# Performance work log

Hardware: AMD Instinct MI355X
Metric: run time of the kernel (lower is better)

Reference implementation:

```python
import jax, jax.numpy as jnp
import numpy as np

N_NODES = 100000
N_EDGES = 1600000
IN_CH = 6
EDGE_FEAT = 8


def glorot(key, shape):
    lim = np.sqrt(6.0 / (shape[0] + shape[1]))
    return jax.random.uniform(key, shape, jnp.float32, -lim, lim)


def setup_inputs() -> dict:
    key = jax.random.key(0)
    ks = jax.random.split(key, 10)
    x = jax.random.normal(ks[0], (N_NODES, IN_CH), jnp.float32)
    edge_index = jax.random.randint(ks[1], (2, N_EDGES), 0, N_NODES, jnp.int64)
    edge_attr = jax.random.normal(ks[2], (N_EDGES, EDGE_FEAT), jnp.float32)
    return {
        "x": x,
        "edge_index": edge_index,
        "edge_attr": edge_attr,
        "W1": glorot(ks[3], (IN_CH, 32)), "b1": jnp.zeros((32,), jnp.float32),
        "W2": glorot(ks[4], (32, 16)), "b2": jnp.zeros((16,), jnp.float32),
        "W3": glorot(ks[5], (16 * 2 + EDGE_FEAT, 32)), "b3": jnp.zeros((32,), jnp.float32),
        "W4": glorot(ks[6], (32, 1)), "b4": jnp.zeros((1,), jnp.float32),
    }


def gcn_conv(x, src, dst, W, b, n_nodes):
    # PyG GCNConv: add self-loops, symmetric deg^{-1/2} normalization,
    # linear transform, scatter-add aggregation over incoming edges, bias.
    h = x @ W  # [N, out]
    deg = jnp.zeros((n_nodes,), h.dtype).at[dst].add(1.0) + 1.0  # +1 self-loop
    dinv = jax.lax.rsqrt(deg)  # [N]
    norm = dinv[src] * dinv[dst]  # [E]
    msg = h[src] * norm[:, None]  # gather + scale
    agg = jnp.zeros_like(h).at[dst].add(msg)
    agg = agg + h * (dinv * dinv)[:, None]  # self-loop term
    return agg + b


def reference(x, edge_index, edge_attr, W1, b1, W2, b2, W3, b3, W4, b4):
    src, dst = edge_index[0], edge_index[1]
    n = x.shape[0]
    h = jax.nn.relu(gcn_conv(x, src, dst, W1, b1, n))
    h = jax.nn.relu(gcn_conv(h, src, dst, W2, b2, n))
    # edge gather-concat-MLP
    edge_input = jnp.concatenate([h[src], h[dst], edge_attr], axis=1)  # [E, 40]
    out = jax.nn.relu(edge_input @ W3 + b3) @ W4 + b4  # [E, 1]
    return out.squeeze(-1)
```

## Files before the change

kernel.cpp:

```cpp
#include <hip/hip_runtime.h>


constexpr int TPB = 256;
constexpr int NB = 256;
constexpr int BSH = 8;
constexpr int MAXB = 1024;
constexpr int EDGE_ITERS = 4;

using short8  = __attribute__((ext_vector_type(8))) short;
using f32x16  = __attribute__((ext_vector_type(16))) float;
using uintx4  = __attribute__((ext_vector_type(4))) unsigned;
using floatx4 = __attribute__((ext_vector_type(4))) float;

__device__ __forceinline__ void nt_store4(uint4 v, uint4* p) {
    uintx4 e = {v.x, v.y, v.z, v.w};
    __builtin_nontemporal_store(e, reinterpret_cast<uintx4*>(p));
}
__device__ __forceinline__ float4 nt_load_f4(const float4* p) {
    floatx4 e = __builtin_nontemporal_load(reinterpret_cast<const floatx4*>(p));
    return float4{e.x, e.y, e.z, e.w};
}

__device__ __forceinline__ float bf_lo(unsigned w) {
    return __builtin_bit_cast(float, (unsigned)(w << 16));
}
__device__ __forceinline__ float bf_hi(unsigned w) {
    return __builtin_bit_cast(float, w & 0xFFFF0000u);
}
__device__ __forceinline__ unsigned bf1(float f) {
    unsigned u = __builtin_bit_cast(unsigned, f);
    return (u + 0x7FFFu + ((u >> 16) & 1u)) >> 16;
}
__device__ __forceinline__ unsigned pk(float lo, float hi) {
    return bf1(lo) | (bf1(hi) << 16);
}
__device__ __forceinline__ void unp8(uint4 v, float* o) {
    o[0] = bf_lo(v.x); o[1] = bf_hi(v.x); o[2] = bf_lo(v.y); o[3] = bf_hi(v.y);
    o[4] = bf_lo(v.z); o[5] = bf_hi(v.z); o[6] = bf_lo(v.w); o[7] = bf_hi(v.w);
}
__device__ __forceinline__ void unp6(uint4 v, float* o) {
    o[0] = bf_lo(v.x); o[1] = bf_hi(v.x); o[2] = bf_lo(v.y); o[3] = bf_hi(v.y);
    o[4] = bf_lo(v.z); o[5] = bf_hi(v.z);
}

__global__ void k_bhist(const int* __restrict__ dst, unsigned* __restrict__ histG,
                        int E, int B, int CH) {
    __shared__ unsigned h[MAXB];
    for (int t = threadIdx.x; t < B; t += blockDim.x) h[t] = 0;
    __syncthreads();
    int b = blockIdx.x;
    int beg = b * CH, end = min(E, beg + CH);
    for (int i = beg + threadIdx.x; i < end; i += blockDim.x)
        atomicAdd(&h[__builtin_nontemporal_load(dst + i) >> BSH], 1u);
    __syncthreads();
    for (int t = threadIdx.x; t < B; t += blockDim.x) histG[b * B + t] = h[t];
}

__global__ void k_scan1t(const unsigned* __restrict__ histG, unsigned* __restrict__ bsum,
                         int M, int B) {
    __shared__ unsigned s[TPB];
    int tid = threadIdx.x;
    int i = blockIdx.x * TPB + tid;
    unsigned v = (i < M) ? histG[(i % NB) * B + (i / NB)] : 0u;
    s[tid] = v;
    __syncthreads();
    for (int ofs = TPB / 2; ofs > 0; ofs >>= 1) {
        if (tid < ofs) s[tid] += s[tid + ofs];
        __syncthreads();
    }
    if (tid == 0) bsum[blockIdx.x] = s[0];
}

__global__ void k_scan2(unsigned* __restrict__ bsum, int nb) {
    __shared__ unsigned s[512];
    int tid = threadIdx.x;
    unsigned v = (tid < nb) ? bsum[tid] : 0u;
    s[tid] = v;
    __syncthreads();
    for (int ofs = 1; ofs < 512; ofs <<= 1) {
        unsigned t = (tid >= ofs) ? s[tid - ofs] : 0u;
        __syncthreads();
        s[tid] += t;
        __syncthreads();
    }
    if (tid < nb) bsum[tid] = s[tid] - v;
}

__global__ void k_scan3t(const unsigned* __restrict__ histG, const unsigned* __restrict__ bsum,
                         unsigned* __restrict__ scannedM, int M, int B) {
    __shared__ unsigned s[TPB];
    int tid = threadIdx.x;
    int i = blockIdx.x * TPB + tid;
    unsigned v = (i < M) ? histG[(i % NB) * B + (i / NB)] : 0u;
    s[tid] = v;
    __syncthreads();
    for (int ofs = 1; ofs < TPB; ofs <<= 1) {
        unsigned t = (tid >= ofs) ? s[tid - ofs] : 0u;
        __syncthreads();
        s[tid] += t;
        __syncthreads();
    }
    if (i < M) scannedM[i] = bsum[blockIdx.x] + s[tid] - v;
}

__global__ void k_bscatter(const int* __restrict__ src, const int* __restrict__ dst,
                           const unsigned* __restrict__ scannedM, unsigned* __restrict__ lvl1,
                           int E, int B, int CH) {
    __shared__ unsigned cur[MAXB];
    int b = blockIdx.x;
    for (int t = threadIdx.x; t < B; t += blockDim.x) cur[t] = scannedM[t * NB + b];
    __syncthreads();
    int beg = b * CH, end = min(E, beg + CH);
    for (int i = beg + threadIdx.x; i < end; i += blockDim.x) {
        int d = __builtin_nontemporal_load(dst + i);
        int sv = __builtin_nontemporal_load(src + i);
        int bk = d >> BSH;
        unsigned p = atomicAdd(&cur[bk], 1u);
        lvl1[p] = ((unsigned)sv << BSH) | (unsigned)(d & ((1 << BSH) - 1));
    }
}

__global__ void k_bbuild(const unsigned* __restrict__ lvl1, const unsigned* __restrict__ scannedM,
                         const float* __restrict__ x, unsigned* __restrict__ rowptr,
                         float* __restrict__ dinv, uint4* __restrict__ xs,
                         int* __restrict__ csr_src, int N, int E, int B) {
    __shared__ unsigned cnt[1 << BSH];
    __shared__ unsigned ro[1 << BSH];
    int b = blockIdx.x;
    int tid = threadIdx.x;
    unsigned gbase = scannedM[(size_t)b * NB];
    unsigned gend = (b + 1 < B) ? scannedM[(size_t)(b + 1) * NB] : (unsigned)E;
    cnt[tid] = 0;
    __syncthreads();
    for (unsigned i = gbase + tid; i < gend; i += (unsigned)blockDim.x)
        atomicAdd(&cnt[lvl1[i] & ((1u << BSH) - 1u)], 1u);
    __syncthreads();
    unsigned v = cnt[tid];
    ro[tid] = v;
    __syncthreads();
    for (int ofs = 1; ofs < (1 << BSH); ofs <<= 1) {
        unsigned t = (tid >= ofs) ? ro[tid - ofs] : 0u;
        __syncthreads();
        ro[tid] += t;
        __syncthreads();
    }
    unsigned excl = ro[tid] - v;
    int n = (b << BSH) + tid;
    if (n < N) {
        rowptr[n] = gbase + excl;
        float di = rsqrtf((float)v + 1.0f);
        dinv[n] = di;
        const float* xr = x + (size_t)n * 6;
        uint4 o;
        o.x = pk(xr[0] * di, xr[1] * di);
        o.y = pk(xr[2] * di, xr[3] * di);
        o.z = pk(xr[4] * di, xr[5] * di);
        o.w = 0u;
        xs[n] = o;
        if (n == N - 1) rowptr[N] = gend;
    }
    __syncthreads();
    cnt[tid] = gbase + excl;
    __syncthreads();
    for (unsigned i = gbase + tid; i < gend; i += (unsigned)blockDim.x) {
        unsigned w = lvl1[i];
        unsigned p = atomicAdd(&cnt[w & ((1u << BSH) - 1u)], 1u);
        csr_src[p] = (int)(w >> BSH);
    }
}

__global__ void k_gagg6f(const unsigned* __restrict__ rowptr, const int* __restrict__ csr_src,
                         const float* __restrict__ dinv, const uint4* __restrict__ xs,
                         const float* __restrict__ W1, const float* __restrict__ b1,
                         const float* __restrict__ W2, uint4* __restrict__ hs2, int N) {
    int gid = blockIdx.x * blockDim.x + threadIdx.x;
    int n = gid >> 2, q = gid & 3;
    if (n >= N) return;
    unsigned beg = rowptr[n], end = rowptr[n + 1];
    float acc[6] = {0.f, 0.f, 0.f, 0.f, 0.f, 0.f};
    for (unsigned j = beg + q; j < end; j += 4) {
        int s = __builtin_nontemporal_load(csr_src + j);
        float t[6];
        unp6(xs[s], t);
#pragma unroll
        for (int i = 0; i < 6; ++i) acc[i] += t[i];
    }
#pragma unroll
    for (int i = 0; i < 6; ++i) {
        acc[i] += __shfl_xor(acc[i], 1);
        acc[i] += __shfl_xor(acc[i], 2);
    }
    float t6[6];
    unp6(xs[n], t6);
#pragma unroll
    for (int i = 0; i < 6; ++i) acc[i] += t6[i];
    float di = dinv[n];
    float h1[8];
#pragma unroll
    for (int cc = 0; cc < 8; ++cc) {
        int oc = q * 8 + cc;
        float s = 0.f;
#pragma unroll
        for (int k = 0; k < 6; ++k) s = fmaf(acc[k], W1[k * 32 + oc], s);
        h1[cc] = fmaxf(fmaf(s, di, b1[oc]), 0.f);
    }
    float z[16];
#pragma unroll
    for (int j = 0; j < 16; ++j) z[j] = 0.f;
#pragma unroll
    for (int cc = 0; cc < 8; ++cc) {
        int c = q * 8 + cc;
        float a = h1[cc];
#pragma unroll
        for (int j = 0; j < 16; ++j) z[j] = fmaf(a, W2[c * 16 + j], z[j]);
    }
#pragma unroll
    for (int j = 0; j < 16; ++j) {
        z[j] += __shfl_xor(z[j], 1);
        z[j] += __shfl_xor(z[j], 2);
    }
    if (q < 2) {
        unsigned w[4];
#pragma unroll
        for (int p = 0; p < 4; ++p)
            w[p] = pk(z[q * 8 + 2 * p] * di, z[q * 8 + 2 * p + 1] * di);
        nt_store4(uint4{w[0], w[1], w[2], w[3]}, hs2 + (size_t)n * 2 + q);
    }
}

__global__ void k_gagg16(const unsigned* __restrict__ rowptr, const int* __restrict__ csr_src,
                         const float* __restrict__ dinv, const uint4* __restrict__ hs2,
                         const float* __restrict__ b2, uint4* __restrict__ h2, int N) {
    int gid = blockIdx.x * blockDim.x + threadIdx.x;
    int n = gid >> 3, q = gid & 7;
    int h = q & 1, e4 = q >> 1;
    if (n >= N) return;
    unsigned beg = rowptr[n], end = rowptr[n + 1];
    float acc[8] = {0.f, 0.f, 0.f, 0.f, 0.f, 0.f, 0.f, 0.f};
    for (unsigned j = beg + e4; j < end; j += 4) {
        int s = __builtin_nontemporal_load(csr_src + j);
        float t[8];
        unp8(hs2[(size_t)s * 2 + h], t);
#pragma unroll
        for (int i = 0; i < 8; ++i) acc[i] += t[i];
    }
#pragma unroll
    for (int i = 0; i < 8; ++i) {
        acc[i] += __shfl_xor(acc[i], 2);
        acc[i] += __shfl_xor(acc[i], 4);
    }
    if (e4) return;
    float t8[8];
    unp8(hs2[(size_t)n * 2 + h], t8);
    float di = dinv[n];
    unsigned w[4];
#pragma unroll
    for (int i = 0; i < 4; ++i) {
        float r0 = fmaxf(fmaf(acc[2 * i] + t8[2 * i], di, b2[h * 8 + 2 * i]), 0.f);
        float r1 = fmaxf(fmaf(acc[2 * i + 1] + t8[2 * i + 1], di, b2[h * 8 + 2 * i + 1]), 0.f);
        w[i] = pk(r0, r1);
    }
    h2[(size_t)n * 2 + h] = uint4{w[0], w[1], w[2], w[3]};
}

__global__ void k_wprep(const float* __restrict__ W3, const float* __restrict__ b3,
                        uint4* __restrict__ w3tab) {
    int lane = threadIdx.x;
    if (lane >= 64) return;
    int j = lane & 31, hi = lane >> 5;
#pragma unroll
    for (int s = 0; s < 3; ++s) {
        unsigned w[4];
#pragma unroll
        for (int p = 0; p < 4; ++p) {
            int k0 = s * 16 + hi * 8 + 2 * p;
            float f0 = (k0 < 40) ? W3[k0 * 32 + j] : (k0 == 40 ? b3[j] : 0.f);
            float f1 = (k0 + 1 < 40) ? W3[(k0 + 1) * 32 + j] : 0.f;
            w[p] = pk(f0, f1);
        }
        w3tab[lane * 3 + s] = uint4{w[0], w[1], w[2], w[3]};
    }
}

__global__ void __launch_bounds__(TPB) k_edge_mfma(
    const int* __restrict__ src, const int* __restrict__ dst,
    const uint4* __restrict__ h2, const float* __restrict__ eattr,
    const uint4* __restrict__ w3tab, const float* __restrict__ W4,
    const float* __restrict__ b4, float* __restrict__ out, int E) {
    const int lane = threadIdx.x & 63;
    const int wave = threadIdx.x >> 6;
    const int e31 = lane & 31;
    const int hi = lane >> 5;

    short8 wA0, wA1, wA2;
    {
        const uint4* wt = w3tab + (size_t)lane * 3;
        wA0 = __builtin_bit_cast(short8, wt[0]);
        wA1 = __builtin_bit_cast(short8, wt[1]);
        wA2 = __builtin_bit_cast(short8, wt[2]);
    }
    const float4* W4v = reinterpret_cast<const float4*>(W4);
    const float4 w4q0 = W4v[hi], w4q1 = W4v[2 + hi], w4q2 = W4v[4 + hi], w4q3 = W4v[6 + hi];
    const float b4v = b4[0];
    const long base0 = ((long)blockIdx.x * 4 + wave) * (32L * EDGE_ITERS);

    const uint4 one_u = (hi == 1) ? uint4{0x3F80u, 0u, 0u, 0u} : uint4{0u, 0u, 0u, 0u};
    const short8 one_s8 = __builtin_bit_cast(short8, one_u);

    auto eclamp = [&](int it) -> size_t {
        long et = base0 + (long)it * 32 + e31;
        return (size_t)(et < E ? et : (long)(E - 1));
    };
    auto load_a2 = [&](int it) -> short8 {
        if (hi != 0) return one_s8;
        const float4* ea = reinterpret_cast<const float4*>(eattr + eclamp(it) * 8);
        float4 e0 = nt_load_f4(ea);
        float4 e1 = nt_load_f4(ea + 1);
        return __builtin_bit_cast(short8, uint4{pk(e0.x, e0.y), pk(e0.z, e0.w),
                                                pk(e1.x, e1.y), pk(e1.z, e1.w)});
    };

    int is[EDGE_ITERS], id[EDGE_ITERS];
#pragma unroll
    for (int it = 0; it < EDGE_ITERS; ++it) {
        is[it] = __builtin_nontemporal_load(src + eclamp(it));
        id[it] = __builtin_nontemporal_load(dst + eclamp(it));
    }

    uint4 hsA = h2[(size_t)is[0] * 2 + hi], hdA = h2[(size_t)id[0] * 2 + hi];
    short8 a2A = load_a2(0);
    uint4 hsB = h2[(size_t)is[1] * 2 + hi], hdB = h2[(size_t)id[1] * 2 + hi];
    short8 a2B = load_a2(1);

#pragma unroll
    for (int it = 0; it < EDGE_ITERS; ++it) {
        uint4 hsC{0u, 0u, 0u, 0u}, hdC{0u, 0u, 0u, 0u};
        short8 a2C = one_s8;
        if (it + 2 < EDGE_ITERS) {
            hsC = h2[(size_t)is[it + 2] * 2 + hi];
            hdC = h2[(size_t)id[it + 2] * 2 + hi];
            a2C = load_a2(it + 2);
        }

        f32x16 c;
#pragma unroll
        for (int i = 0; i < 16; ++i) c[i] = 0.f;
        c = __builtin_amdgcn_mfma_f32_32x32x16_bf16(wA0, __builtin_bit_cast(short8, hsA), c, 0, 0, 0);
        c = __builtin_amdgcn_mfma_f32_32x32x16_bf16(wA1, __builtin_bit_cast(short8, hdA), c, 0, 0, 0);
        c = __builtin_amdgcn_mfma_f32_32x32x16_bf16(wA2, a2A, c, 0, 0, 0);

        float z = 0.f;
#pragma unroll
        for (int r = 0; r < 4; ++r) {
            z = fmaf(fmaxf(c[0 * 4 + r], 0.f), ((const float*)&w4q0)[r], z);
            z = fmaf(fmaxf(c[1 * 4 + r], 0.f), ((const float*)&w4q1)[r], z);
            z = fmaf(fmaxf(c[2 * 4 + r], 0.f), ((const float*)&w4q2)[r], z);
            z = fmaf(fmaxf(c[3 * 4 + r], 0.f), ((const float*)&w4q3)[r], z);
        }
        z += __shfl_xor(z, 32);
        long erow = base0 + (long)it * 32 + e31;
        if (hi == 0 && erow < E) __builtin_nontemporal_store(z + b4v, out + erow);

        hsA = hsB; hdA = hdB; a2A = a2B;
        hsB = hsC; hdB = hdC; a2B = a2C;
    }
}

extern "C" void kernel_launch(void* const* d_in, const int* in_sizes, int n_in,
                              void* d_out, int out_size, void* d_ws, size_t ws_size,
                              hipStream_t stream) {
    const float* x     = (const float*)d_in[0];
    const int*   ei    = (const int*)d_in[1];
    const float* eattr = (const float*)d_in[2];
    const float* W1 = (const float*)d_in[3];
    const float* b1 = (const float*)d_in[4];
    const float* W2 = (const float*)d_in[5];
    const float* b2 = (const float*)d_in[6];
    const float* W3 = (const float*)d_in[7];
    const float* b3 = (const float*)d_in[8];
    const float* W4 = (const float*)d_in[9];
    const float* b4 = (const float*)d_in[10];
    float* out = (float*)d_out;

    const int N = in_sizes[0] / 6;
    const int E = in_sizes[2] / 8;
    const int* src = ei;
    const int* dst = ei + E;

    const int B  = (N + (1 << BSH) - 1) >> BSH;
    const int CH = (E + NB - 1) / NB;
    const int M  = B * NB;
    const int nbM = (M + TPB - 1) / TPB;

    char* wsb = (char*)d_ws;
    size_t off = 0;
    auto alloc4 = [&](size_t elems) {
        void* p = wsb + off;
        off += ((elems * 4 + 15) & ~(size_t)15);
        return p;
    };
    unsigned* rowptr   = (unsigned*)alloc4(N + 1);
    float*    dinv     = (float*)alloc4(N);
    unsigned* bsum     = (unsigned*)alloc4(512);
    unsigned* histG    = (unsigned*)alloc4((size_t)NB * B);
    unsigned* scannedM = (unsigned*)alloc4((size_t)NB * B);
    int*      csr_src  = (int*)alloc4(E);
    unsigned* big      = (unsigned*)alloc4((size_t)N * 16 > (size_t)E ? (size_t)N * 16 : (size_t)E);
    uint4*    xs       = (uint4*)alloc4((size_t)N * 4);
    uint4*    w3tab    = (uint4*)alloc4(64 * 3 * 4);

    unsigned* lvl1 = big;
    uint4*    hs2  = (uint4*)big;
    uint4*    h2   = (uint4*)(big + (size_t)N * 8);

    k_wprep<<<1, 64, 0, stream>>>(W3, b3, w3tab);

    k_bhist   <<<NB, TPB, 0, stream>>>(dst, histG, E, B, CH);
    k_scan1t  <<<nbM, TPB, 0, stream>>>(histG, bsum, M, B);
    k_scan2   <<<1, 512, 0, stream>>>(bsum, nbM);
    k_scan3t  <<<nbM, TPB, 0, stream>>>(histG, bsum, scannedM, M, B);
    k_bscatter<<<NB, TPB, 0, stream>>>(src, dst, scannedM, lvl1, E, B, CH);
    k_bbuild  <<<B, 1 << BSH, 0, stream>>>(lvl1, scannedM, x, rowptr, dinv, xs, csr_src, N, E, B);

    k_gagg6f<<<((size_t)N * 4 + TPB - 1) / TPB, TPB, 0, stream>>>(
        rowptr, csr_src, dinv, xs, W1, b1, W2, hs2, N);

    k_gagg16<<<((size_t)N * 8 + TPB - 1) / TPB, TPB, 0, stream>>>(
        rowptr, csr_src, dinv, hs2, b2, h2, N);

    const long per_block = 4L * 32 * EDGE_ITERS;
    const int eblocks = (int)((E + per_block - 1) / per_block);
    k_edge_mfma<<<eblocks, TPB, 0, stream>>>(src, dst, (const uint4*)h2, eattr,
                                             (const uint4*)w3tab, W4, b4, out, E);
}
```

Measured before the change: 172.3 us.

## Software-pipeline gathers in GCN aggregation and use persistent edge MLP waves

Both GCN aggregation kernels now prefetch the next CSR index two steps ahead and the next gathered feature row one step ahead, with clamped indices, so gather latency overlaps accumulation. The edge MFMA kernel switches from a fixed 4 tiles per wave to a fixed grid of 2048 blocks, where each wave loops over a computed number of tiles with a rolling one-ahead prefetch of indices, features and edge attributes. This is meant to hide memory latency and cut block launch overhead. In exchange it adds extra clamped loads at loop tails and a shallower prefetch depth in the edge kernel.

After: 178.0 us. 1.03x slower.

```diff
diff --git a/kernel.cpp b/kernel.cpp
--- a/kernel.cpp
+++ b/kernel.cpp
@@ -5,7 +5,6 @@
 constexpr int NB = 256;
 constexpr int BSH = 8;
 constexpr int MAXB = 1024;
-constexpr int EDGE_ITERS = 4;
 
 using short8  = __attribute__((ext_vector_type(8))) short;
 using f32x16  = __attribute__((ext_vector_type(16))) float;
@@ -172,18 +171,28 @@
 __global__ void k_gagg6f(const unsigned* __restrict__ rowptr, const int* __restrict__ csr_src,
                          const float* __restrict__ dinv, const uint4* __restrict__ xs,
                          const float* __restrict__ W1, const float* __restrict__ b1,
-                         const float* __restrict__ W2, uint4* __restrict__ hs2, int N) {
+                         const float* __restrict__ W2, uint4* __restrict__ hs2, int N, int E) {
     int gid = blockIdx.x * blockDim.x + threadIdx.x;
     int n = gid >> 2, q = gid & 3;
     if (n >= N) return;
     unsigned beg = rowptr[n], end = rowptr[n + 1];
     float acc[6] = {0.f, 0.f, 0.f, 0.f, 0.f, 0.f};
-    for (unsigned j = beg + q; j < end; j += 4) {
-        int s = __builtin_nontemporal_load(csr_src + j);
-        float t[6];
-        unp6(xs[s], t);
-#pragma unroll
-        for (int i = 0; i < 6; ++i) acc[i] += t[i];
+    unsigned j0 = beg + q;
+    if (j0 < end) {
+        auto cidx = [&](unsigned jj) {
+            return __builtin_nontemporal_load(csr_src + (jj < end ? jj : end - 1));
+        };
+        int i1 = cidx(j0 + 4);
+        uint4 g0 = xs[cidx(j0)];
+        for (unsigned j = j0; j < end; j += 4) {
+            int i2 = cidx(j + 8);
+            uint4 g1 = xs[i1];
+            float t[6];
+            unp6(g0, t);
+#pragma unroll
+            for (int i = 0; i < 6; ++i) acc[i] += t[i];
+            g0 = g1; i1 = i2;
+        }
     }
 #pragma unroll
     for (int i = 0; i < 6; ++i) {
@@ -230,19 +239,29 @@
 
 __global__ void k_gagg16(const unsigned* __restrict__ rowptr, const int* __restrict__ csr_src,
                          const float* __restrict__ dinv, const uint4* __restrict__ hs2,
-                         const float* __restrict__ b2, uint4* __restrict__ h2, int N) {
+                         const float* __restrict__ b2, uint4* __restrict__ h2, int N, int E) {
     int gid = blockIdx.x * blockDim.x + threadIdx.x;
     int n = gid >> 3, q = gid & 7;
     int h = q & 1, e4 = q >> 1;
     if (n >= N) return;
     unsigned beg = rowptr[n], end = rowptr[n + 1];
     float acc[8] = {0.f, 0.f, 0.f, 0.f, 0.f, 0.f, 0.f, 0.f};
-    for (unsigned j = beg + e4; j < end; j += 4) {
-        int s = __builtin_nontemporal_load(csr_src + j);
-        float t[8];
-        unp8(hs2[(size_t)s * 2 + h], t);
-#pragma unroll
-        for (int i = 0; i < 8; ++i) acc[i] += t[i];
+    unsigned j0 = beg + e4;
+    if (j0 < end) {
+        auto cidx = [&](unsigned jj) {
+            return __builtin_nontemporal_load(csr_src + (jj < end ? jj : end - 1));
+        };
+        int i1 = cidx(j0 + 4);
+        uint4 g0 = hs2[(size_t)cidx(j0) * 2 + h];
+        for (unsigned j = j0; j < end; j += 4) {
+            int i2 = cidx(j + 8);
+            uint4 g1 = hs2[(size_t)i1 * 2 + h];
+            float t[8];
+            unp8(g0, t);
+#pragma unroll
+            for (int i = 0; i < 8; ++i) acc[i] += t[i];
+            g0 = g1; i1 = i2;
+        }
     }
 #pragma unroll
     for (int i = 0; i < 8; ++i) {
@@ -286,7 +305,7 @@
     const int* __restrict__ src, const int* __restrict__ dst,
     const uint4* __restrict__ h2, const float* __restrict__ eattr,
     const uint4* __restrict__ w3tab, const float* __restrict__ W4,
-    const float* __restrict__ b4, float* __restrict__ out, int E) {
+    const float* __restrict__ b4, float* __restrict__ out, int E, int tpw) {
     const int lane = threadIdx.x & 63;
     const int wave = threadIdx.x >> 6;
     const int e31 = lane & 31;
@@ -302,7 +321,8 @@
     const float4* W4v = reinterpret_cast<const float4*>(W4);
     const float4 w4q0 = W4v[hi], w4q1 = W4v[2 + hi], w4q2 = W4v[4 + hi], w4q3 = W4v[6 + hi];
     const float b4v = b4[0];
-    const long base0 = ((long)blockIdx.x * 4 + wave) * (32L * EDGE_ITERS);
+    const long gw = (long)blockIdx.x * 4 + wave;
+    const long base0 = gw * tpw * 32L;
 
     const uint4 one_u = (hi == 1) ? uint4{0x3F80u, 0u, 0u, 0u} : uint4{0u, 0u, 0u, 0u};
     const short8 one_s8 = __builtin_bit_cast(short8, one_u);
@@ -320,34 +340,26 @@
                                                 pk(e1.x, e1.y), pk(e1.z, e1.w)});
     };
 
-    int is[EDGE_ITERS], id[EDGE_ITERS];
-#pragma unroll
-    for (int it = 0; it < EDGE_ITERS; ++it) {
-        is[it] = __builtin_nontemporal_load(src + eclamp(it));
-        id[it] = __builtin_nontemporal_load(dst + eclamp(it));
-    }
-
-    uint4 hsA = h2[(size_t)is[0] * 2 + hi], hdA = h2[(size_t)id[0] * 2 + hi];
-    short8 a2A = load_a2(0);
-    uint4 hsB = h2[(size_t)is[1] * 2 + hi], hdB = h2[(size_t)id[1] * 2 + hi];
-    short8 a2B = load_a2(1);
-
-#pragma unroll
-    for (int it = 0; it < EDGE_ITERS; ++it) {
-        uint4 hsC{0u, 0u, 0u, 0u}, hdC{0u, 0u, 0u, 0u};
-        short8 a2C = one_s8;
-        if (it + 2 < EDGE_ITERS) {
-            hsC = h2[(size_t)is[it + 2] * 2 + hi];
-            hdC = h2[(size_t)id[it + 2] * 2 + hi];
-            a2C = load_a2(it + 2);
-        }
+    int is1 = __builtin_nontemporal_load(src + eclamp(0));
+    int id1 = __builtin_nontemporal_load(dst + eclamp(0));
+    int is2 = __builtin_nontemporal_load(src + eclamp(1));
+    int id2 = __builtin_nontemporal_load(dst + eclamp(1));
+    uint4 hs0 = h2[(size_t)is1 * 2 + hi], hd0 = h2[(size_t)id1 * 2 + hi];
+    short8 a20 = load_a2(0);
+    is1 = is2; id1 = id2;
+
+    for (int it = 0; it < tpw; ++it) {
+        is2 = __builtin_nontemporal_load(src + eclamp(it + 2));
+        id2 = __builtin_nontemporal_load(dst + eclamp(it + 2));
+        uint4 hs1 = h2[(size_t)is1 * 2 + hi], hd1 = h2[(size_t)id1 * 2 + hi];
+        short8 a21 = load_a2(it + 1);
 
         f32x16 c;
 #pragma unroll
         for (int i = 0; i < 16; ++i) c[i] = 0.f;
-        c = __builtin_amdgcn_mfma_f32_32x32x16_bf16(wA0, __builtin_bit_cast(short8, hsA), c, 0, 0, 0);
-        c = __builtin_amdgcn_mfma_f32_32x32x16_bf16(wA1, __builtin_bit_cast(short8, hdA), c, 0, 0, 0);
-        c = __builtin_amdgcn_mfma_f32_32x32x16_bf16(wA2, a2A, c, 0, 0, 0);
+        c = __builtin_amdgcn_mfma_f32_32x32x16_bf16(wA0, __builtin_bit_cast(short8, hs0), c, 0, 0, 0);
+        c = __builtin_amdgcn_mfma_f32_32x32x16_bf16(wA1, __builtin_bit_cast(short8, hd0), c, 0, 0, 0);
+        c = __builtin_amdgcn_mfma_f32_32x32x16_bf16(wA2, a20, c, 0, 0, 0);
 
         float z = 0.f;
 #pragma unroll
@@ -361,8 +373,8 @@
         long erow = base0 + (long)it * 32 + e31;
         if (hi == 0 && erow < E) __builtin_nontemporal_store(z + b4v, out + erow);
 
-        hsA = hsB; hdA = hdB; a2A = a2B;
-        hsB = hsC; hdB = hdC; a2B = a2C;
+        hs0 = hs1; hd0 = hd1; a20 = a21;
+        is1 = is2; id1 = id2;
     }
 }
 
@@ -423,13 +435,15 @@
     k_bbuild  <<<B, 1 << BSH, 0, stream>>>(lvl1, scannedM, x, rowptr, dinv, xs, csr_src, N, E, B);
 
     k_gagg6f<<<((size_t)N * 4 + TPB - 1) / TPB, TPB, 0, stream>>>(
-        rowptr, csr_src, dinv, xs, W1, b1, W2, hs2, N);
+        rowptr, csr_src, dinv, xs, W1, b1, W2, hs2, N, E);
 
     k_gagg16<<<((size_t)N * 8 + TPB - 1) / TPB, TPB, 0, stream>>>(
-        rowptr, csr_src, dinv, hs2, b2, h2, N);
-
-    const long per_block = 4L * 32 * EDGE_ITERS;
-    const int eblocks = (int)((E + per_block - 1) / per_block);
+        rowptr, csr_src, dinv, hs2, b2, h2, N, E);
+
+    const int eblocks = 2048;
+    const int ntiles = (E + 31) / 32;
+    const int totalw = eblocks * 4;
+    const int tpw = (ntiles + totalw - 1) / totalw;
     k_edge_mfma<<<eblocks, TPB, 0, stream>>>(src, dst, (const uint4*)h2, eattr,
-                                             (const uint4*)w3tab, W4, b4, out, E);
-}
+                                             (const uint4*)w3tab, W4, b4, out, E, tpw);
+}
```
